# Optimization experiments

Hardware: AMD Instinct MI355X
Metric: run time of the kernel (lower is better)

The kernel has to match this reference:

```python
import jax, jax.numpy as jnp
import numpy as np

E, H, I, G, T, TOPK = 8, 2048, 5632, 128, 256, 2
FP8_MAX = 448.0


def setup_inputs() -> dict:
    key = jax.random.key(0)
    ks = jax.random.split(key, 8)
    hidden_states = jax.random.normal(ks[0], (T, H), jnp.float32)
    router_logits = jax.random.normal(ks[1], (T, E), jnp.float32)
    # unpacked INT4 values in [-8, 7], stored as int8 (modeling unpack_int4->int8)
    w3w1_q = jax.random.randint(ks[2], (E, H, 2 * I), -8, 8, dtype=jnp.int32).astype(jnp.int8)
    w2_q = jax.random.randint(ks[3], (E, I, H), -8, 8, dtype=jnp.int32).astype(jnp.int8)
    # group-wise weight scales: [in_dim/G, out_dim] per expert
    w3w1_scale = jax.random.uniform(ks[4], (E, H // G, 2 * I), jnp.float32, 0.005, 0.02)
    w2_scale = jax.random.uniform(ks[5], (E, I // G, H), jnp.float32, 0.005, 0.02)
    # per-expert static activation scales (p3_p1 = max(p1,p3) pre-folded)
    input_scale_fc1 = jax.random.uniform(ks[6], (E,), jnp.float32, 0.5, 1.5)
    input_scale_fc2 = jax.random.uniform(ks[7], (E,), jnp.float32, 0.5, 1.5)
    return dict(hidden_states=hidden_states, router_logits=router_logits,
                w3w1_q=w3w1_q, w2_q=w2_q, w3w1_scale=w3w1_scale, w2_scale=w2_scale,
                input_scale_fc1=input_scale_fc1, input_scale_fc2=input_scale_fc2)


def _fp8_qdq(x, s):
    # quantize activation to fp8_e4m3 (clamp + round-to-fp8) then dequantize
    q = jnp.clip(x / s, -FP8_MAX, FP8_MAX).astype(jnp.float8_e4m3fn)
    return q.astype(jnp.float32)


def _dequant(w_q, w_scale):
    # w_q: [in, out] int8; w_scale: [in/G, out] -> repeat each group G rows
    return w_q.astype(jnp.float32) * jnp.repeat(w_scale, G, axis=0)


def _routing(router_logits):
    probs = jax.nn.softmax(router_logits, axis=-1)            # [T, E]
    vals, idx = jax.lax.top_k(probs, TOPK)                    # [T, K]
    scales = vals / jnp.sum(vals, axis=-1, keepdims=True)     # renormalize
    # per-token gate weight for every expert, zero if not selected: [T, E]
    gate = jnp.sum(jax.nn.one_hot(idx, E, dtype=scales.dtype) * scales[..., None], axis=1)
    return gate


def reference(hidden_states, router_logits, w3w1_q, w2_q, w3w1_scale, w2_scale,
              input_scale_fc1, input_scale_fc2):
    gate = _routing(router_logits)                            # [T, E]
    out = jnp.zeros_like(hidden_states)
    for e in range(E):  # fixed small expert loop (structurally distinct weights)
        s1 = input_scale_fc1[e]
        act = _fp8_qdq(hidden_states, s1)                     # [T, H]
        w_fc1 = _dequant(w3w1_q[e], w3w1_scale[e])            # [H, 2I]
        fc1 = (act @ w_fc1) * s1                              # [T, 2I]
        up, gt = fc1[:, :I], fc1[:, I:]                       # chunk: (w3 | w1)
        h = up * jax.nn.silu(gt)                              # [T, I]
        s2 = input_scale_fc2[e]
        act2 = _fp8_qdq(h, s2)
        w_fc2 = _dequant(w2_q[e], w2_scale[e])                # [I, H]
        fc2 = (act2 @ w_fc2) * s2                             # [T, H]
        out = out + fc2 * gate[:, e:e + 1]
    return out
```

## Files before the change

### kernel.cpp

```cpp
#include <hip/hip_runtime.h>
#include <hip/hip_bf16.h>
#include <hip/hip_fp8.h>
#include <cstdint>
#include <cstddef>

#define E_ 8
#define H_ 2048
#define I_ 5632
#define N1_ (2 * I_)
#define G_ 128
#define T_ 256
#define RPE 256
#define SLOTS (E_ * RPE)

typedef __attribute__((ext_vector_type(4))) float f32x4;
typedef __attribute__((ext_vector_type(8))) __bf16 bf16x8;
typedef __attribute__((ext_vector_type(2))) int i32x2;

#define WS_CNT 0
#define WS_TOKEN 64
#define WS_GATE (64 + SLOTS * 4)
#define WS_A1 32768
#define WS_A2 (WS_A1 + SLOTS * H_ * 2)

__device__ __forceinline__ uint32_t pack_bf16x2(float a, float b) {
  union { float f; uint32_t u; } ua, ub;
  ua.f = a; ub.f = b;
  uint32_t ra = (ua.u + 0x7FFFu + ((ua.u >> 16) & 1u)) >> 16;
  uint32_t rb = (ub.u + 0x7FFFu + ((ub.u >> 16) & 1u)) & 0xFFFF0000u;
  return ra | rb;
}

__device__ __forceinline__ float fp8_qdq1(float x) {
  x = fminf(fmaxf(x, -448.0f), 448.0f);
  __hip_fp8_e4m3 q(x);
  return (float)q;
}

__device__ __forceinline__ void block_sync_nodrain() {
  __builtin_amdgcn_sched_barrier(0);
  asm volatile("s_waitcnt lgkmcnt(0)" ::: "memory");
  __builtin_amdgcn_s_barrier();
  __builtin_amdgcn_sched_barrier(0);
}

__device__ __forceinline__ void wissue(const int* __restrict__ wpt, size_t ldN, int m,
                                       i32x2 wv[4]) {
#pragma unroll
  for (int c = 0; c < 4; ++c)
    wv[c] = __builtin_nontemporal_load(
        reinterpret_cast<const i32x2*>(wpt + ((size_t)m * 32 + c) * ldN));
}

__device__ __forceinline__ void wstage(__hip_bfloat16 (*Btb)[64][8], int kqw, int n0, int h4,
                                       const i32x2 wv[4], float2 sc) {
  uint32_t a0 = pack_bf16x2((float)wv[0].x * sc.x, (float)wv[1].x * sc.x);
  uint32_t a1 = pack_bf16x2((float)wv[2].x * sc.x, (float)wv[3].x * sc.x);
  uint32_t b0 = pack_bf16x2((float)wv[0].y * sc.y, (float)wv[1].y * sc.y);
  uint32_t b1 = pack_bf16x2((float)wv[2].y * sc.y, (float)wv[3].y * sc.y);
  *(uint2*)&Btb[kqw][n0][h4] = make_uint2(a0, a1);
  *(uint2*)&Btb[kqw][n0 + 1][h4] = make_uint2(b0, b1);
}

__device__ __forceinline__ void aissue(const __hip_bfloat16* const aptr[4], int m, int nact,
                                       uint4 av[4]) {
#pragma unroll
  for (int mj = 0; mj < 4; ++mj)
    if (mj < nact) av[mj] = *(const uint4*)(aptr[mj] + (size_t)m * 32);
}

__device__ __forceinline__ void do_mfma(const __hip_bfloat16 (*Btb)[64][8], int kq, int lm,
                                        int nact, const uint4 afr[4], f32x4 acc[4][4]) {
#pragma unroll
  for (int f = 0; f < 4; ++f) {
    union { uint4 u; bf16x8 v; } bu;
    bu.u = *(const uint4*)&Btb[kq][f * 16 + lm][0];
#pragma unroll
    for (int mj = 0; mj < 4; ++mj)
      if (mj < nact) {
        union { uint4 u; bf16x8 v; } au;
        au.u = afr[mj];
        acc[mj][f] = __builtin_amdgcn_mfma_f32_16x16x32_bf16(au.v, bu.v, acc[mj][f], 0, 0, 0);
      }
  }
}

__global__ void routing_kernel(const float* __restrict__ logits,
                               int* __restrict__ cnt,
                               int* __restrict__ token_of, float* __restrict__ gate_of) {
  __shared__ int s_cnt[E_];
  int t = threadIdx.x;
  if (t < E_) s_cnt[t] = 0;
  __syncthreads();
  float l[E_];
#pragma unroll
  for (int e = 0; e < E_; e++) l[e] = logits[t * E_ + e];
  int i0 = 0;
#pragma unroll
  for (int e = 1; e < E_; e++) if (l[e] > l[i0]) i0 = e;
  int i1 = (i0 == 0) ? 1 : 0;
#pragma unroll
  for (int e = 0; e < E_; e++) if (e != i0 && l[e] > l[i1]) i1 = e;
  float g0 = 1.0f / (1.0f + expf(l[i1] - l[i0]));
  float g1 = 1.0f - g0;
  int s0 = atomicAdd(&s_cnt[i0], 1);
  int s1 = atomicAdd(&s_cnt[i1], 1);
  token_of[i0 * RPE + s0] = t;  gate_of[i0 * RPE + s0] = g0;
  token_of[i1 * RPE + s1] = t;  gate_of[i1 * RPE + s1] = g1;
  __syncthreads();
  if (t < E_) cnt[t] = s_cnt[t];
  for (int idx = t; idx < SLOTS; idx += 256) {
    int e = idx >> 8, r = idx & (RPE - 1);
    if (r >= s_cnt[e]) { token_of[idx] = 0; gate_of[idx] = 0.0f; }
  }
}

__global__ void gather_kernel(const float* __restrict__ hidden,
                              const float* __restrict__ is1,
                              const int* __restrict__ cnt,
                              const int* __restrict__ token_of,
                              __hip_bfloat16* __restrict__ A1) {
  int sg = blockIdx.x;
  int e = sg >> 8, r = sg & (RPE - 1);
  bool pad = (r >= cnt[e]);
  uint4 u;
  if (pad) {
    u.x = u.y = u.z = u.w = 0u;
  } else {
    int t = token_of[sg];
    float s1 = is1[e];
    const float4* hp = (const float4*)(hidden + (size_t)t * H_ + threadIdx.x * 8);
    float4 x0 = hp[0], x1 = hp[1];
    float q0 = fp8_qdq1(x0.x / s1), q1 = fp8_qdq1(x0.y / s1);
    float q2 = fp8_qdq1(x0.z / s1), q3 = fp8_qdq1(x0.w / s1);
    float q4 = fp8_qdq1(x1.x / s1), q5 = fp8_qdq1(x1.y / s1);
    float q6 = fp8_qdq1(x1.z / s1), q7 = fp8_qdq1(x1.w / s1);
    u.x = pack_bf16x2(q0, q1); u.y = pack_bf16x2(q2, q3);
    u.z = pack_bf16x2(q4, q5); u.w = pack_bf16x2(q6, q7);
  }
  ((uint4*)(A1 + (size_t)sg * H_))[threadIdx.x] = u;
}

__global__ __launch_bounds__(256) void fc1_kernel(
    const int* __restrict__ w1, const float* __restrict__ w1s,
    const float* __restrict__ is1v, const float* __restrict__ is2v,
    const int* __restrict__ cnt,
    const __hip_bfloat16* __restrict__ A1, __hip_bfloat16* __restrict__ A2) {
  __shared__ __hip_bfloat16 Bt[2][4][64][8];
  const int e = blockIdx.y;
  const int j0 = blockIdx.x * 32;
  const int tid = threadIdx.x;
  const int wave = tid >> 6, lane = tid & 63;
  const int lm = lane & 15, kq = lane >> 4;
  const int np = tid & 31, kg = tid >> 5;
  const int kqw = kg >> 1, h4 = (kg & 1) * 4;
  const int n0s = np * 2;
  const int gc2 = (n0s < 32) ? (j0 + n0s) : (I_ + j0 + (n0s - 32));
  const int* wpt = w1 + (size_t)e * H_ * N1_ + (size_t)(kg * 4) * N1_ + gc2;
  const float* spt = w1s + (size_t)e * (H_ / G_) * N1_ + gc2;
  const __hip_bfloat16* abase = A1 + (size_t)e * RPE * H_;

  const int C16 = (cnt[e] + 15) >> 4;
  int nact = (C16 - wave + 3) >> 2;
  if (nact < 0) nact = 0;

  f32x4 acc[4][4];
#pragma unroll
  for (int a = 0; a < 4; a++)
#pragma unroll
    for (int b = 0; b < 4; b++) acc[a][b] = (f32x4){0.f, 0.f, 0.f, 0.f};

  const __hip_bfloat16* aptr[4];
#pragma unroll
  for (int mj = 0; mj < 4; mj++)
    aptr[mj] = abase + (size_t)((mj * 4 + wave) * 16 + lm) * H_ + kq * 8;

  i32x2 wv0[4], wv1[4];
  uint4 av0[4], av1[4];
  float2 sc0 = *(const float2*)spt;
  float2 sc1 = sc0;
  wissue(wpt, N1_, 0, wv0);
  wissue(wpt, N1_, 1, wv1);
  aissue(aptr, 0, nact, av1);
  wstage(Bt[0], kqw, n0s, h4, wv0, sc0);
  block_sync_nodrain();

  for (int i = 0; i < 31; ++i) {
    const int ks = 2 * i;
    if (((ks + 2) & 3) == 0) sc0 = *(const float2*)(spt + (size_t)((ks + 2) >> 2) * N1_);
    wissue(wpt, N1_, ks + 2, wv0);
    aissue(aptr, ks + 1, nact, av0);
    do_mfma(Bt[0], kq, lm, nact, av1, acc);
    wstage(Bt[1], kqw, n0s, h4, wv1, sc1);
    block_sync_nodrain();
    if (((ks + 3) & 3) == 1) sc1 = *(const float2*)(spt + (size_t)((ks + 3) >> 2) * N1_);
    wissue(wpt, N1_, ks + 3, wv1);
    aissue(aptr, ks + 2, nact, av1);
    do_mfma(Bt[1], kq, lm, nact, av0, acc);
    wstage(Bt[0], kqw, n0s, h4, wv0, sc0);
    block_sync_nodrain();
  }
  aissue(aptr, 63, nact, av0);
  do_mfma(Bt[0], kq, lm, nact, av1, acc);
  wstage(Bt[1], kqw, n0s, h4, wv1, sc1);
  block_sync_nodrain();
  do_mfma(Bt[1], kq, lm, nact, av0, acc);

  const float s1 = is1v[e], s2 = is2v[e];
  __hip_bfloat16* a2base = A2 + (size_t)(e * RPE) * I_ + j0;
#pragma unroll
  for (int mj = 0; mj < 4; mj++) {
    if (mj < nact) {
      int mrow = (mj * 4 + wave) * 16 + kq * 4;
#pragma unroll
      for (int r = 0; r < 4; r++) {
#pragma unroll
        for (int f = 0; f < 2; f++) {
          float up = acc[mj][f][r] * s1;
          float gt = acc[mj][f + 2][r] * s1;
          float h = up * (gt / (1.0f + expf(-gt)));
          float q = fp8_qdq1(h / s2);
          a2base[(size_t)(mrow + r) * I_ + f * 16 + lm] = __float2bfloat16(q);
        }
      }
    }
  }
}

__global__ __launch_bounds__(256) void fc2_kernel(
    const int* __restrict__ w2, const float* __restrict__ w2s,
    const float* __restrict__ is2v, const int* __restrict__ cnt,
    const int* __restrict__ token_of, const float* __restrict__ gate_of,
    const __hip_bfloat16* __restrict__ A2, float* __restrict__ out) {
  __shared__ __hip_bfloat16 Bt[2][4][64][8];
  const int e = blockIdx.y;
  const int n0 = blockIdx.x * 64;
  const int z = blockIdx.z;
  const int tid = threadIdx.x;
  const int wave = tid >> 6, lane = tid & 63;
  const int lm = lane & 15, kq = lane >> 4;
  const int np = tid & 31, kg = tid >> 5;
  const int kqw = kg >> 1, h4 = (kg & 1) * 4;
  const int n0s = np * 2;
  const int gc2 = n0 + n0s;
  const int z11 = z * 11;
  const int* wpt = w2 + (size_t)e * I_ * H_ + (size_t)(z * 44 * 32 + kg * 4) * H_ + gc2;
  const float* spt = w2s + (size_t)e * (I_ / G_) * H_ + gc2;
  const __hip_bfloat16* abase = A2 + (size_t)e * RPE * I_;

  const int c_n = cnt[e];
  const int C16 = (c_n + 15) >> 4;
  int nact = (C16 - wave + 3) >> 2;
  if (nact < 0) nact = 0;

  f32x4 acc[4][4];
#pragma unroll
  for (int a = 0; a < 4; a++)
#pragma unroll
    for (int b = 0; b < 4; b++) acc[a][b] = (f32x4){0.f, 0.f, 0.f, 0.f};

  const __hip_bfloat16* aptr[4];
#pragma unroll
  for (int mj = 0; mj < 4; mj++)
    aptr[mj] = abase + (size_t)((mj * 4 + wave) * 16 + lm) * I_ + (size_t)z * 44 * 32 + kq * 8;

  i32x2 wv0[4], wv1[4];
  uint4 av0[4], av1[4];
  float2 sc0 = *(const float2*)(spt + (size_t)z11 * H_);
  float2 sc1 = sc0;
  wissue(wpt, H_, 0, wv0);
  wissue(wpt, H_, 1, wv1);
  aissue(aptr, 0, nact, av1);
  wstage(Bt[0], kqw, n0s, h4, wv0, sc0);
  block_sync_nodrain();

  for (int i = 0; i < 21; ++i) {
    const int ks = 2 * i;
    if (((ks + 2) & 3) == 0)
      sc0 = *(const float2*)(spt + (size_t)(z11 + ((ks + 2) >> 2)) * H_);
    wissue(wpt, H_, ks + 2, wv0);
    aissue(aptr, ks + 1, nact, av0);
    do_mfma(Bt[0], kq, lm, nact, av1, acc);
    wstage(Bt[1], kqw, n0s, h4, wv1, sc1);
    block_sync_nodrain();
    if (((ks + 3) & 3) == 1)
      sc1 = *(const float2*)(spt + (size_t)(z11 + ((ks + 3) >> 2)) * H_);
    wissue(wpt, H_, ks + 3, wv1);
    aissue(aptr, ks + 2, nact, av1);
    do_mfma(Bt[1], kq, lm, nact, av0, acc);
    wstage(Bt[0], kqw, n0s, h4, wv0, sc0);
    block_sync_nodrain();
  }
  aissue(aptr, 43, nact, av0);
  do_mfma(Bt[0], kq, lm, nact, av1, acc);
  wstage(Bt[1], kqw, n0s, h4, wv1, sc1);
  block_sync_nodrain();
  do_mfma(Bt[1], kq, lm, nact, av0, acc);

  const float s2 = is2v[e];
#pragma unroll
  for (int mj = 0; mj < 4; mj++) {
    if (mj < nact) {
      int sl0 = (mj * 4 + wave) * 16 + kq * 4;
#pragma unroll
      for (int r = 0; r < 4; r++) {
        int slot = sl0 + r;
        if (slot < c_n) {
          int t = token_of[e * RPE + slot];
          float gv = gate_of[e * RPE + slot] * s2;
#pragma unroll
          for (int f = 0; f < 4; f++)
            atomicAdd(out + (size_t)t * H_ + n0 + f * 16 + lm, acc[mj][f][r] * gv);
        }
      }
    }
  }
}

extern "C" void kernel_launch(void* const* d_in, const int* in_sizes, int n_in,
                              void* d_out, int out_size, void* d_ws, size_t ws_size,
                              hipStream_t stream) {
  const float* hidden = (const float*)d_in[0];
  const float* logits = (const float*)d_in[1];
  const int* w1 = (const int*)d_in[2];
  const int* w2 = (const int*)d_in[3];
  const float* w1s = (const float*)d_in[4];
  const float* w2s = (const float*)d_in[5];
  const float* is1 = (const float*)d_in[6];
  const float* is2 = (const float*)d_in[7];
  float* out = (float*)d_out;
  char* ws = (char*)d_ws;
  int* cnt = (int*)(ws + WS_CNT);
  int* token_of = (int*)(ws + WS_TOKEN);
  float* gate_of = (float*)(ws + WS_GATE);
  __hip_bfloat16* A1 = (__hip_bfloat16*)(ws + WS_A1);
  __hip_bfloat16* A2 = (__hip_bfloat16*)(ws + WS_A2);

  hipMemsetAsync(d_out, 0, (size_t)T_ * H_ * sizeof(float), stream);
  routing_kernel<<<1, 256, 0, stream>>>(logits, cnt, token_of, gate_of);
  gather_kernel<<<SLOTS, 256, 0, stream>>>(hidden, is1, cnt, token_of, A1);
  fc1_kernel<<<dim3(I_ / 32, E_), 256, 0, stream>>>(w1, w1s, is1, is2, cnt, A1, A2);
  fc2_kernel<<<dim3(H_ / 64, E_, 4), 256, 0, stream>>>(w2, w2s, is2, cnt, token_of,
                                                       gate_of, A2, out);
}
```

Measured before the change: 1.242 ms.

## Give each wave its own weight tile to drop block barriers in FC kernels

The FC1 and FC2 kernels are restructured so each wave dequantizes and stages its own private slice of weight columns (16-byte loads, per-wave LDS buffers) and covers all token rows itself. This removes the block-wide barriers in the K loop and doubles the columns per block. The aim is to cut barrier stalls and improve weight load width. In exchange, A loads are repeated across waves and register pressure rises with 8x2 accumulators. The gather kernel also skips writing padded rows beyond the last 16-row tile.

```diff
diff --git a/kernel.cpp b/kernel.cpp
--- a/kernel.cpp
+++ b/kernel.cpp
@@ -15,7 +15,7 @@
 
 typedef __attribute__((ext_vector_type(4))) float f32x4;
 typedef __attribute__((ext_vector_type(8))) __bf16 bf16x8;
-typedef __attribute__((ext_vector_type(2))) int i32x2;
+typedef __attribute__((ext_vector_type(4))) int i32x4;
 
 #define WS_CNT 0
 #define WS_TOKEN 64
@@ -37,49 +37,42 @@
   return (float)q;
 }
 
-__device__ __forceinline__ void block_sync_nodrain() {
-  __builtin_amdgcn_sched_barrier(0);
-  asm volatile("s_waitcnt lgkmcnt(0)" ::: "memory");
-  __builtin_amdgcn_s_barrier();
-  __builtin_amdgcn_sched_barrier(0);
-}
-
-__device__ __forceinline__ void wissue(const int* __restrict__ wpt, size_t ldN, int m,
-                                       i32x2 wv[4]) {
+__device__ __forceinline__ void wissue4(const int* __restrict__ wpt, size_t ldN, int m,
+                                        i32x4 wv[4]) {
 #pragma unroll
   for (int c = 0; c < 4; ++c)
     wv[c] = __builtin_nontemporal_load(
-        reinterpret_cast<const i32x2*>(wpt + ((size_t)m * 32 + c) * ldN));
-}
-
-__device__ __forceinline__ void wstage(__hip_bfloat16 (*Btb)[64][8], int kqw, int n0, int h4,
-                                       const i32x2 wv[4], float2 sc) {
-  uint32_t a0 = pack_bf16x2((float)wv[0].x * sc.x, (float)wv[1].x * sc.x);
-  uint32_t a1 = pack_bf16x2((float)wv[2].x * sc.x, (float)wv[3].x * sc.x);
-  uint32_t b0 = pack_bf16x2((float)wv[0].y * sc.y, (float)wv[1].y * sc.y);
-  uint32_t b1 = pack_bf16x2((float)wv[2].y * sc.y, (float)wv[3].y * sc.y);
-  *(uint2*)&Btb[kqw][n0][h4] = make_uint2(a0, a1);
-  *(uint2*)&Btb[kqw][n0 + 1][h4] = make_uint2(b0, b1);
-}
-
-__device__ __forceinline__ void aissue(const __hip_bfloat16* const aptr[4], int m, int nact,
-                                       uint4 av[4]) {
-#pragma unroll
-  for (int mj = 0; mj < 4; ++mj)
+        reinterpret_cast<const i32x4*>(wpt + ((size_t)m * 32 + c) * ldN));
+}
+
+__device__ __forceinline__ void wstage4(__hip_bfloat16 (*Btb)[32][8], int kqw, int c4, int s0,
+                                        const i32x4 wv[4], f32x4 sc) {
+#pragma unroll
+  for (int i = 0; i < 4; ++i) {
+    uint32_t p0 = pack_bf16x2((float)wv[0][i] * sc[i], (float)wv[1][i] * sc[i]);
+    uint32_t p1 = pack_bf16x2((float)wv[2][i] * sc[i], (float)wv[3][i] * sc[i]);
+    *(uint2*)&Btb[kqw][c4 + i][s0] = make_uint2(p0, p1);
+  }
+}
+
+__device__ __forceinline__ void aissue8(const __hip_bfloat16* const aptr[8], int m, int nact,
+                                        uint4 av[8]) {
+#pragma unroll
+  for (int mj = 0; mj < 8; ++mj)
     if (mj < nact) av[mj] = *(const uint4*)(aptr[mj] + (size_t)m * 32);
 }
 
-__device__ __forceinline__ void do_mfma(const __hip_bfloat16 (*Btb)[64][8], int kq, int lm,
-                                        int nact, const uint4 afr[4], f32x4 acc[4][4]) {
-#pragma unroll
-  for (int f = 0; f < 4; ++f) {
+__device__ __forceinline__ void mfma2x8(const __hip_bfloat16 (*Btb)[32][8], int kq, int lm,
+                                        int nact, const uint4 av[8], f32x4 acc[8][2]) {
+#pragma unroll
+  for (int f = 0; f < 2; ++f) {
     union { uint4 u; bf16x8 v; } bu;
     bu.u = *(const uint4*)&Btb[kq][f * 16 + lm][0];
 #pragma unroll
-    for (int mj = 0; mj < 4; ++mj)
+    for (int mj = 0; mj < 8; ++mj)
       if (mj < nact) {
         union { uint4 u; bf16x8 v; } au;
-        au.u = afr[mj];
+        au.u = av[mj];
         acc[mj][f] = __builtin_amdgcn_mfma_f32_16x16x32_bf16(au.v, bu.v, acc[mj][f], 0, 0, 0);
       }
   }
@@ -122,7 +115,10 @@
                               __hip_bfloat16* __restrict__ A1) {
   int sg = blockIdx.x;
   int e = sg >> 8, r = sg & (RPE - 1);
-  bool pad = (r >= cnt[e]);
+  int c_n = cnt[e];
+  int lim = ((c_n + 15) >> 4) << 4;
+  if (r >= lim) return;
+  bool pad = (r >= c_n);
   uint4 u;
   if (pad) {
     u.x = u.y = u.z = u.w = 0u;
@@ -141,176 +137,170 @@
   ((uint4*)(A1 + (size_t)sg * H_))[threadIdx.x] = u;
 }
 
-__global__ __launch_bounds__(256) void fc1_kernel(
+__global__ __launch_bounds__(256, 2) void fc1_kernel(
     const int* __restrict__ w1, const float* __restrict__ w1s,
     const float* __restrict__ is1v, const float* __restrict__ is2v,
     const int* __restrict__ cnt,
     const __hip_bfloat16* __restrict__ A1, __hip_bfloat16* __restrict__ A2) {
-  __shared__ __hip_bfloat16 Bt[2][4][64][8];
+  __shared__ __hip_bfloat16 Bt[4][2][4][32][8];
   const int e = blockIdx.y;
-  const int j0 = blockIdx.x * 32;
+  const int j0 = blockIdx.x * 64;
   const int tid = threadIdx.x;
   const int wave = tid >> 6, lane = tid & 63;
   const int lm = lane & 15, kq = lane >> 4;
-  const int np = tid & 31, kg = tid >> 5;
-  const int kqw = kg >> 1, h4 = (kg & 1) * 4;
-  const int n0s = np * 2;
-  const int gc2 = (n0s < 32) ? (j0 + n0s) : (I_ + j0 + (n0s - 32));
-  const int* wpt = w1 + (size_t)e * H_ * N1_ + (size_t)(kg * 4) * N1_ + gc2;
-  const float* spt = w1s + (size_t)e * (H_ / G_) * N1_ + gc2;
+  const int c4 = (lane & 7) * 4;
+  const int kq4 = lane >> 3;
+  const int kqw = kq4 >> 1, s0 = (kq4 & 1) * 4;
+  const int gc4 = (c4 < 16) ? (j0 + wave * 16 + c4) : (I_ + j0 + wave * 16 + (c4 - 16));
+  const int* wpt = w1 + (size_t)e * H_ * N1_ + (size_t)(kq4 * 4) * N1_ + gc4;
+  const float* spt = w1s + (size_t)e * (H_ / G_) * N1_ + gc4;
   const __hip_bfloat16* abase = A1 + (size_t)e * RPE * H_;
+  auto& Btw = Bt[wave];
 
   const int C16 = (cnt[e] + 15) >> 4;
-  int nact = (C16 - wave + 3) >> 2;
-  if (nact < 0) nact = 0;
-
-  f32x4 acc[4][4];
-#pragma unroll
-  for (int a = 0; a < 4; a++)
-#pragma unroll
-    for (int b = 0; b < 4; b++) acc[a][b] = (f32x4){0.f, 0.f, 0.f, 0.f};
-
-  const __hip_bfloat16* aptr[4];
-#pragma unroll
-  for (int mj = 0; mj < 4; mj++)
-    aptr[mj] = abase + (size_t)((mj * 4 + wave) * 16 + lm) * H_ + kq * 8;
-
-  i32x2 wv0[4], wv1[4];
-  uint4 av0[4], av1[4];
-  float2 sc0 = *(const float2*)spt;
-  float2 sc1 = sc0;
-  wissue(wpt, N1_, 0, wv0);
-  wissue(wpt, N1_, 1, wv1);
-  aissue(aptr, 0, nact, av1);
-  wstage(Bt[0], kqw, n0s, h4, wv0, sc0);
-  block_sync_nodrain();
-
-  for (int i = 0; i < 31; ++i) {
-    const int ks = 2 * i;
-    if (((ks + 2) & 3) == 0) sc0 = *(const float2*)(spt + (size_t)((ks + 2) >> 2) * N1_);
-    wissue(wpt, N1_, ks + 2, wv0);
-    aissue(aptr, ks + 1, nact, av0);
-    do_mfma(Bt[0], kq, lm, nact, av1, acc);
-    wstage(Bt[1], kqw, n0s, h4, wv1, sc1);
-    block_sync_nodrain();
-    if (((ks + 3) & 3) == 1) sc1 = *(const float2*)(spt + (size_t)((ks + 3) >> 2) * N1_);
-    wissue(wpt, N1_, ks + 3, wv1);
-    aissue(aptr, ks + 2, nact, av1);
-    do_mfma(Bt[1], kq, lm, nact, av0, acc);
-    wstage(Bt[0], kqw, n0s, h4, wv0, sc0);
-    block_sync_nodrain();
-  }
-  aissue(aptr, 63, nact, av0);
-  do_mfma(Bt[0], kq, lm, nact, av1, acc);
-  wstage(Bt[1], kqw, n0s, h4, wv1, sc1);
-  block_sync_nodrain();
-  do_mfma(Bt[1], kq, lm, nact, av0, acc);
-
   const float s1 = is1v[e], s2 = is2v[e];
-  __hip_bfloat16* a2base = A2 + (size_t)(e * RPE) * I_ + j0;
-#pragma unroll
-  for (int mj = 0; mj < 4; mj++) {
-    if (mj < nact) {
-      int mrow = (mj * 4 + wave) * 16 + kq * 4;
-#pragma unroll
-      for (int r = 0; r < 4; r++) {
-#pragma unroll
-        for (int f = 0; f < 2; f++) {
-          float up = acc[mj][f][r] * s1;
-          float gt = acc[mj][f + 2][r] * s1;
+  __hip_bfloat16* a2base = A2 + (size_t)(e * RPE) * I_ + j0 + wave * 16;
+
+  for (int mb = 0; mb < C16; mb += 8) {
+    const int nact = (C16 - mb < 8) ? (C16 - mb) : 8;
+    const __hip_bfloat16* aptr[8];
+#pragma unroll
+    for (int mj = 0; mj < 8; ++mj)
+      aptr[mj] = abase + (size_t)((mb + mj) * 16 + lm) * H_ + kq * 8;
+
+    f32x4 acc[8][2];
+#pragma unroll
+    for (int a = 0; a < 8; ++a)
+#pragma unroll
+      for (int b = 0; b < 2; ++b) acc[a][b] = (f32x4){0.f, 0.f, 0.f, 0.f};
+
+    i32x4 wv0[4], wv1[4];
+    uint4 av0[8], av1[8];
+    f32x4 sc0 = *(const f32x4*)spt;
+    f32x4 sc1 = sc0;
+    wissue4(wpt, N1_, 0, wv0);
+    wissue4(wpt, N1_, 1, wv1);
+    aissue8(aptr, 0, nact, av1);
+    wstage4(&Btw[0][0], kqw, c4, s0, wv0, sc0);
+
+    for (int i = 0; i < 31; ++i) {
+      const int m = 2 * i;
+      if (((m + 2) & 3) == 0) sc0 = *(const f32x4*)(spt + (size_t)((m + 2) >> 2) * N1_);
+      wissue4(wpt, N1_, m + 2, wv0);
+      aissue8(aptr, m + 1, nact, av0);
+      mfma2x8(&Btw[0][0], kq, lm, nact, av1, acc);
+      wstage4(&Btw[1][0], kqw, c4, s0, wv1, sc1);
+      if (((m + 3) & 3) == 1) sc1 = *(const f32x4*)(spt + (size_t)((m + 3) >> 2) * N1_);
+      wissue4(wpt, N1_, m + 3, wv1);
+      aissue8(aptr, m + 2, nact, av1);
+      mfma2x8(&Btw[1][0], kq, lm, nact, av0, acc);
+      wstage4(&Btw[0][0], kqw, c4, s0, wv0, sc0);
+    }
+    aissue8(aptr, 63, nact, av0);
+    mfma2x8(&Btw[0][0], kq, lm, nact, av1, acc);
+    wstage4(&Btw[1][0], kqw, c4, s0, wv1, sc1);
+    mfma2x8(&Btw[1][0], kq, lm, nact, av0, acc);
+
+#pragma unroll
+    for (int mj = 0; mj < 8; ++mj) {
+      if (mj < nact) {
+        int mrow = (mb + mj) * 16 + kq * 4;
+#pragma unroll
+        for (int r = 0; r < 4; ++r) {
+          float up = acc[mj][0][r] * s1;
+          float gt = acc[mj][1][r] * s1;
           float h = up * (gt / (1.0f + expf(-gt)));
           float q = fp8_qdq1(h / s2);
-          a2base[(size_t)(mrow + r) * I_ + f * 16 + lm] = __float2bfloat16(q);
+          a2base[(size_t)(mrow + r) * I_ + lm] = __float2bfloat16(q);
         }
       }
     }
   }
 }
 
-__global__ __launch_bounds__(256) void fc2_kernel(
+__global__ __launch_bounds__(256, 2) void fc2_kernel(
     const int* __restrict__ w2, const float* __restrict__ w2s,
     const float* __restrict__ is2v, const int* __restrict__ cnt,
     const int* __restrict__ token_of, const float* __restrict__ gate_of,
     const __hip_bfloat16* __restrict__ A2, float* __restrict__ out) {
-  __shared__ __hip_bfloat16 Bt[2][4][64][8];
+  __shared__ __hip_bfloat16 Bt[4][2][4][32][8];
   const int e = blockIdx.y;
-  const int n0 = blockIdx.x * 64;
+  const int n0 = blockIdx.x * 128;
   const int z = blockIdx.z;
   const int tid = threadIdx.x;
   const int wave = tid >> 6, lane = tid & 63;
   const int lm = lane & 15, kq = lane >> 4;
-  const int np = tid & 31, kg = tid >> 5;
-  const int kqw = kg >> 1, h4 = (kg & 1) * 4;
-  const int n0s = np * 2;
-  const int gc2 = n0 + n0s;
-  const int z11 = z * 11;
-  const int* wpt = w2 + (size_t)e * I_ * H_ + (size_t)(z * 44 * 32 + kg * 4) * H_ + gc2;
-  const float* spt = w2s + (size_t)e * (I_ / G_) * H_ + gc2;
-  const __hip_bfloat16* abase = A2 + (size_t)e * RPE * I_;
+  const int c4 = (lane & 7) * 4;
+  const int kq4 = lane >> 3;
+  const int kqw = kq4 >> 1, s0 = (kq4 & 1) * 4;
+  const int gc4 = n0 + wave * 32 + c4;
+  const int* wpt = w2 + (size_t)e * I_ * H_ + (size_t)(z * 1408 + kq4 * 4) * H_ + gc4;
+  const float* spt = w2s + (size_t)e * (I_ / G_) * H_ + gc4;
+  const __hip_bfloat16* abase = A2 + (size_t)e * RPE * I_ + z * 1408;
+  auto& Btw = Bt[wave];
 
   const int c_n = cnt[e];
   const int C16 = (c_n + 15) >> 4;
-  int nact = (C16 - wave + 3) >> 2;
-  if (nact < 0) nact = 0;
-
-  f32x4 acc[4][4];
-#pragma unroll
-  for (int a = 0; a < 4; a++)
-#pragma unroll
-    for (int b = 0; b < 4; b++) acc[a][b] = (f32x4){0.f, 0.f, 0.f, 0.f};
-
-  const __hip_bfloat16* aptr[4];
-#pragma unroll
-  for (int mj = 0; mj < 4; mj++)
-    aptr[mj] = abase + (size_t)((mj * 4 + wave) * 16 + lm) * I_ + (size_t)z * 44 * 32 + kq * 8;
-
-  i32x2 wv0[4], wv1[4];
-  uint4 av0[4], av1[4];
-  float2 sc0 = *(const float2*)(spt + (size_t)z11 * H_);
-  float2 sc1 = sc0;
-  wissue(wpt, H_, 0, wv0);
-  wissue(wpt, H_, 1, wv1);
-  aissue(aptr, 0, nact, av1);
-  wstage(Bt[0], kqw, n0s, h4, wv0, sc0);
-  block_sync_nodrain();
-
-  for (int i = 0; i < 21; ++i) {
-    const int ks = 2 * i;
-    if (((ks + 2) & 3) == 0)
-      sc0 = *(const float2*)(spt + (size_t)(z11 + ((ks + 2) >> 2)) * H_);
-    wissue(wpt, H_, ks + 2, wv0);
-    aissue(aptr, ks + 1, nact, av0);
-    do_mfma(Bt[0], kq, lm, nact, av1, acc);
-    wstage(Bt[1], kqw, n0s, h4, wv1, sc1);
-    block_sync_nodrain();
-    if (((ks + 3) & 3) == 1)
-      sc1 = *(const float2*)(spt + (size_t)(z11 + ((ks + 3) >> 2)) * H_);
-    wissue(wpt, H_, ks + 3, wv1);
-    aissue(aptr, ks + 2, nact, av1);
-    do_mfma(Bt[1], kq, lm, nact, av0, acc);
-    wstage(Bt[0], kqw, n0s, h4, wv0, sc0);
-    block_sync_nodrain();
-  }
-  aissue(aptr, 43, nact, av0);
-  do_mfma(Bt[0], kq, lm, nact, av1, acc);
-  wstage(Bt[1], kqw, n0s, h4, wv1, sc1);
-  block_sync_nodrain();
-  do_mfma(Bt[1], kq, lm, nact, av0, acc);
-
+  const int z11 = z * 11;
   const float s2 = is2v[e];
-#pragma unroll
-  for (int mj = 0; mj < 4; mj++) {
-    if (mj < nact) {
-      int sl0 = (mj * 4 + wave) * 16 + kq * 4;
-#pragma unroll
-      for (int r = 0; r < 4; r++) {
-        int slot = sl0 + r;
-        if (slot < c_n) {
-          int t = token_of[e * RPE + slot];
-          float gv = gate_of[e * RPE + slot] * s2;
-#pragma unroll
-          for (int f = 0; f < 4; f++)
-            atomicAdd(out + (size_t)t * H_ + n0 + f * 16 + lm, acc[mj][f][r] * gv);
+
+  for (int mb = 0; mb < C16; mb += 8) {
+    const int nact = (C16 - mb < 8) ? (C16 - mb) : 8;
+    const __hip_bfloat16* aptr[8];
+#pragma unroll
+    for (int mj = 0; mj < 8; ++mj)
+      aptr[mj] = abase + (size_t)((mb + mj) * 16 + lm) * I_ + kq * 8;
+
+    f32x4 acc[8][2];
+#pragma unroll
+    for (int a = 0; a < 8; ++a)
+#pragma unroll
+      for (int b = 0; b < 2; ++b) acc[a][b] = (f32x4){0.f, 0.f, 0.f, 0.f};
+
+    i32x4 wv0[4], wv1[4];
+    uint4 av0[8], av1[8];
+    f32x4 sc0 = *(const f32x4*)(spt + (size_t)z11 * H_);
+    f32x4 sc1 = sc0;
+    wissue4(wpt, H_, 0, wv0);
+    wissue4(wpt, H_, 1, wv1);
+    aissue8(aptr, 0, nact, av1);
+    wstage4(&Btw[0][0], kqw, c4, s0, wv0, sc0);
+
+    for (int i = 0; i < 21; ++i) {
+      const int m = 2 * i;
+      if (((m + 2) & 3) == 0)
+        sc0 = *(const f32x4*)(spt + (size_t)(z11 + ((m + 2) >> 2)) * H_);
+      wissue4(wpt, H_, m + 2, wv0);
+      aissue8(aptr, m + 1, nact, av0);
+      mfma2x8(&Btw[0][0], kq, lm, nact, av1, acc);
+      wstage4(&Btw[1][0], kqw, c4, s0, wv1, sc1);
+      if (((m + 3) & 3) == 1)
+        sc1 = *(const f32x4*)(spt + (size_t)(z11 + ((m + 3) >> 2)) * H_);
+      wissue4(wpt, H_, m + 3, wv1);
+      aissue8(aptr, m + 2, nact, av1);
+      mfma2x8(&Btw[1][0], kq, lm, nact, av0, acc);
+      wstage4(&Btw[0][0], kqw, c4, s0, wv0, sc0);
+    }
+    aissue8(aptr, 43, nact, av0);
+    mfma2x8(&Btw[0][0], kq, lm, nact, av1, acc);
+    wstage4(&Btw[1][0], kqw, c4, s0, wv1, sc1);
+    mfma2x8(&Btw[1][0], kq, lm, nact, av0, acc);
+
+#pragma unroll
+    for (int mj = 0; mj < 8; ++mj) {
+      if (mj < nact) {
+        int sl0 = (mb + mj) * 16 + kq * 4;
+#pragma unroll
+        for (int r = 0; r < 4; ++r) {
+          int slot = sl0 + r;
+          if (slot < c_n) {
+            int t = token_of[e * RPE + slot];
+            float gv = gate_of[e * RPE + slot] * s2;
+#pragma unroll
+            for (int f = 0; f < 2; ++f)
+              atomicAdd(out + (size_t)t * H_ + n0 + wave * 32 + f * 16 + lm,
+                        acc[mj][f][r] * gv);
+          }
         }
       }
     }
@@ -339,7 +329,7 @@
   hipMemsetAsync(d_out, 0, (size_t)T_ * H_ * sizeof(float), stream);
   routing_kernel<<<1, 256, 0, stream>>>(logits, cnt, token_of, gate_of);
   gather_kernel<<<SLOTS, 256, 0, stream>>>(hidden, is1, cnt, token_of, A1);
-  fc1_kernel<<<dim3(I_ / 32, E_), 256, 0, stream>>>(w1, w1s, is1, is2, cnt, A1, A2);
-  fc2_kernel<<<dim3(H_ / 64, E_, 4), 256, 0, stream>>>(w2, w2s, is2, cnt, token_of,
-                                                       gate_of, A2, out);
-}
+  fc1_kernel<<<dim3(I_ / 64, E_), 256, 0, stream>>>(w1, w1s, is1, is2, cnt, A1, A2);
+  fc2_kernel<<<dim3(H_ / 128, E_, 4), 256, 0, stream>>>(w2, w2s, is2, cnt, token_of,
+                                                        gate_of, A2, out);
+}
```

Result: slower. 1.326 ms (+6.7%).

## Widen weight loads to 16 bytes and deepen weight prefetch to four stages

Applied to the files above, without the earlier changes.

In fc1 and fc2, each thread now loads four adjacent int32 weight columns per row as 128-bit nontemporal loads over two rows, replacing the earlier 64-bit loads over four rows. The k-loop is unrolled by four with four register buffers, so weight loads are issued about four k-steps before they are used and the group scale is loaded once per group as a float4. The aim is fewer, wider memory requests and more loads in flight, which should hide HBM latency on this weight-bandwidth-bound GEMM. The gather kernel also returns early for padded rows past the 16-aligned count, skipping writes that are never read. The cost is higher register pressure from the extra buffers and a new LDS store pattern that writes 32-bit elements, which may cause bank conflicts.

```diff
diff --git a/kernel.cpp b/kernel.cpp
--- a/kernel.cpp
+++ b/kernel.cpp
@@ -15,7 +15,7 @@
 
 typedef __attribute__((ext_vector_type(4))) float f32x4;
 typedef __attribute__((ext_vector_type(8))) __bf16 bf16x8;
-typedef __attribute__((ext_vector_type(2))) int i32x2;
+typedef __attribute__((ext_vector_type(4))) int i32x4;
 
 #define WS_CNT 0
 #define WS_TOKEN 64
@@ -45,21 +45,20 @@
 }
 
 __device__ __forceinline__ void wissue(const int* __restrict__ wpt, size_t ldN, int m,
-                                       i32x2 wv[4]) {
-#pragma unroll
-  for (int c = 0; c < 4; ++c)
-    wv[c] = __builtin_nontemporal_load(
-        reinterpret_cast<const i32x2*>(wpt + ((size_t)m * 32 + c) * ldN));
-}
-
-__device__ __forceinline__ void wstage(__hip_bfloat16 (*Btb)[64][8], int kqw, int n0, int h4,
-                                       const i32x2 wv[4], float2 sc) {
-  uint32_t a0 = pack_bf16x2((float)wv[0].x * sc.x, (float)wv[1].x * sc.x);
-  uint32_t a1 = pack_bf16x2((float)wv[2].x * sc.x, (float)wv[3].x * sc.x);
-  uint32_t b0 = pack_bf16x2((float)wv[0].y * sc.y, (float)wv[1].y * sc.y);
-  uint32_t b1 = pack_bf16x2((float)wv[2].y * sc.y, (float)wv[3].y * sc.y);
-  *(uint2*)&Btb[kqw][n0][h4] = make_uint2(a0, a1);
-  *(uint2*)&Btb[kqw][n0 + 1][h4] = make_uint2(b0, b1);
+                                       i32x4 wv[2]) {
+  wv[0] = __builtin_nontemporal_load(
+      reinterpret_cast<const i32x4*>(wpt + ((size_t)m * 32) * ldN));
+  wv[1] = __builtin_nontemporal_load(
+      reinterpret_cast<const i32x4*>(wpt + ((size_t)m * 32 + 1) * ldN));
+}
+
+__device__ __forceinline__ void wstage(__hip_bfloat16 (*Btb)[64][8], int kqs, int c4, int s0,
+                                       const i32x4 wv[2], f32x4 sc) {
+#pragma unroll
+  for (int i = 0; i < 4; ++i) {
+    uint32_t p = pack_bf16x2((float)wv[0][i] * sc[i], (float)wv[1][i] * sc[i]);
+    *(uint32_t*)&Btb[kqs][c4 + i][s0] = p;
+  }
 }
 
 __device__ __forceinline__ void aissue(const __hip_bfloat16* const aptr[4], int m, int nact,
@@ -122,7 +121,10 @@
                               __hip_bfloat16* __restrict__ A1) {
   int sg = blockIdx.x;
   int e = sg >> 8, r = sg & (RPE - 1);
-  bool pad = (r >= cnt[e]);
+  int c_n = cnt[e];
+  int lim = ((c_n + 15) >> 4) << 4;
+  if (r >= lim) return;
+  bool pad = (r >= c_n);
   uint4 u;
   if (pad) {
     u.x = u.y = u.z = u.w = 0u;
@@ -152,12 +154,12 @@
   const int tid = threadIdx.x;
   const int wave = tid >> 6, lane = tid & 63;
   const int lm = lane & 15, kq = lane >> 4;
-  const int np = tid & 31, kg = tid >> 5;
-  const int kqw = kg >> 1, h4 = (kg & 1) * 4;
-  const int n0s = np * 2;
-  const int gc2 = (n0s < 32) ? (j0 + n0s) : (I_ + j0 + (n0s - 32));
-  const int* wpt = w1 + (size_t)e * H_ * N1_ + (size_t)(kg * 4) * N1_ + gc2;
-  const float* spt = w1s + (size_t)e * (H_ / G_) * N1_ + gc2;
+  const int c4 = (tid & 15) * 4;
+  const int r2 = tid >> 4;
+  const int kqs = r2 >> 2, s0 = (r2 * 2) & 7;
+  const int gc4 = (c4 < 32) ? (j0 + c4) : (I_ + j0 + (c4 - 32));
+  const int* wpt = w1 + (size_t)e * H_ * N1_ + (size_t)(r2 * 2) * N1_ + gc4;
+  const float* spt = w1s + (size_t)e * (H_ / G_) * N1_ + gc4;
   const __hip_bfloat16* abase = A1 + (size_t)e * RPE * H_;
 
   const int C16 = (cnt[e] + 15) >> 4;
@@ -175,36 +177,43 @@
   for (int mj = 0; mj < 4; mj++)
     aptr[mj] = abase + (size_t)((mj * 4 + wave) * 16 + lm) * H_ + kq * 8;
 
-  i32x2 wv0[4], wv1[4];
+  i32x4 wvA[2], wvB[2], wvC[2], wvD[2];
   uint4 av0[4], av1[4];
-  float2 sc0 = *(const float2*)spt;
-  float2 sc1 = sc0;
-  wissue(wpt, N1_, 0, wv0);
-  wissue(wpt, N1_, 1, wv1);
+  f32x4 scCur = *(const f32x4*)spt;
+  wissue(wpt, N1_, 0, wvA);
+  wissue(wpt, N1_, 1, wvB);
+  wissue(wpt, N1_, 2, wvC);
+  wissue(wpt, N1_, 3, wvD);
   aissue(aptr, 0, nact, av1);
-  wstage(Bt[0], kqw, n0s, h4, wv0, sc0);
+  wstage(Bt[0], kqs, c4, s0, wvA, scCur);
   block_sync_nodrain();
 
-  for (int i = 0; i < 31; ++i) {
-    const int ks = 2 * i;
-    if (((ks + 2) & 3) == 0) sc0 = *(const float2*)(spt + (size_t)((ks + 2) >> 2) * N1_);
-    wissue(wpt, N1_, ks + 2, wv0);
-    aissue(aptr, ks + 1, nact, av0);
+  for (int it = 0; it < 16; ++it) {
+    const int m = it * 4;
+    f32x4 scN = scCur;
+    if (it + 1 < 16) scN = *(const f32x4*)(spt + (size_t)(it + 1) * N1_);
+    if (m + 4 < 64) wissue(wpt, N1_, m + 4, wvA);
+    if (m + 1 < 64) aissue(aptr, m + 1, nact, av0);
     do_mfma(Bt[0], kq, lm, nact, av1, acc);
-    wstage(Bt[1], kqw, n0s, h4, wv1, sc1);
-    block_sync_nodrain();
-    if (((ks + 3) & 3) == 1) sc1 = *(const float2*)(spt + (size_t)((ks + 3) >> 2) * N1_);
-    wissue(wpt, N1_, ks + 3, wv1);
-    aissue(aptr, ks + 2, nact, av1);
+    wstage(Bt[1], kqs, c4, s0, wvB, scCur);
+    block_sync_nodrain();
+    if (m + 5 < 64) wissue(wpt, N1_, m + 5, wvB);
+    if (m + 2 < 64) aissue(aptr, m + 2, nact, av1);
     do_mfma(Bt[1], kq, lm, nact, av0, acc);
-    wstage(Bt[0], kqw, n0s, h4, wv0, sc0);
-    block_sync_nodrain();
-  }
-  aissue(aptr, 63, nact, av0);
-  do_mfma(Bt[0], kq, lm, nact, av1, acc);
-  wstage(Bt[1], kqw, n0s, h4, wv1, sc1);
-  block_sync_nodrain();
-  do_mfma(Bt[1], kq, lm, nact, av0, acc);
+    wstage(Bt[0], kqs, c4, s0, wvC, scCur);
+    block_sync_nodrain();
+    if (m + 6 < 64) wissue(wpt, N1_, m + 6, wvC);
+    if (m + 3 < 64) aissue(aptr, m + 3, nact, av0);
+    do_mfma(Bt[0], kq, lm, nact, av1, acc);
+    wstage(Bt[1], kqs, c4, s0, wvD, scCur);
+    block_sync_nodrain();
+    if (m + 7 < 64) wissue(wpt, N1_, m + 7, wvD);
+    if (m + 4 < 64) aissue(aptr, m + 4, nact, av1);
+    do_mfma(Bt[1], kq, lm, nact, av0, acc);
+    if (m + 4 < 64) wstage(Bt[0], kqs, c4, s0, wvA, scN);
+    block_sync_nodrain();
+    scCur = scN;
+  }
 
   const float s1 = is1v[e], s2 = is2v[e];
   __hip_bfloat16* a2base = A2 + (size_t)(e * RPE) * I_ + j0;
@@ -239,14 +248,14 @@
   const int tid = threadIdx.x;
   const int wave = tid >> 6, lane = tid & 63;
   const int lm = lane & 15, kq = lane >> 4;
-  const int np = tid & 31, kg = tid >> 5;
-  const int kqw = kg >> 1, h4 = (kg & 1) * 4;
-  const int n0s = np * 2;
-  const int gc2 = n0 + n0s;
+  const int c4 = (tid & 15) * 4;
+  const int r2 = tid >> 4;
+  const int kqs = r2 >> 2, s0 = (r2 * 2) & 7;
+  const int gc4 = n0 + c4;
   const int z11 = z * 11;
-  const int* wpt = w2 + (size_t)e * I_ * H_ + (size_t)(z * 44 * 32 + kg * 4) * H_ + gc2;
-  const float* spt = w2s + (size_t)e * (I_ / G_) * H_ + gc2;
-  const __hip_bfloat16* abase = A2 + (size_t)e * RPE * I_;
+  const int* wpt = w2 + (size_t)e * I_ * H_ + (size_t)(z * 1408 + r2 * 2) * H_ + gc4;
+  const float* spt = w2s + (size_t)e * (I_ / G_) * H_ + gc4;
+  const __hip_bfloat16* abase = A2 + (size_t)e * RPE * I_ + z * 1408;
 
   const int c_n = cnt[e];
   const int C16 = (c_n + 15) >> 4;
@@ -262,40 +271,45 @@
   const __hip_bfloat16* aptr[4];
 #pragma unroll
   for (int mj = 0; mj < 4; mj++)
-    aptr[mj] = abase + (size_t)((mj * 4 + wave) * 16 + lm) * I_ + (size_t)z * 44 * 32 + kq * 8;
-
-  i32x2 wv0[4], wv1[4];
+    aptr[mj] = abase + (size_t)((mj * 4 + wave) * 16 + lm) * I_ + kq * 8;
+
+  i32x4 wvA[2], wvB[2], wvC[2], wvD[2];
   uint4 av0[4], av1[4];
-  float2 sc0 = *(const float2*)(spt + (size_t)z11 * H_);
-  float2 sc1 = sc0;
-  wissue(wpt, H_, 0, wv0);
-  wissue(wpt, H_, 1, wv1);
+  f32x4 scCur = *(const f32x4*)(spt + (size_t)z11 * H_);
+  wissue(wpt, H_, 0, wvA);
+  wissue(wpt, H_, 1, wvB);
+  wissue(wpt, H_, 2, wvC);
+  wissue(wpt, H_, 3, wvD);
   aissue(aptr, 0, nact, av1);
-  wstage(Bt[0], kqw, n0s, h4, wv0, sc0);
+  wstage(Bt[0], kqs, c4, s0, wvA, scCur);
   block_sync_nodrain();
 
-  for (int i = 0; i < 21; ++i) {
-    const int ks = 2 * i;
-    if (((ks + 2) & 3) == 0)
-      sc0 = *(const float2*)(spt + (size_t)(z11 + ((ks + 2) >> 2)) * H_);
-    wissue(wpt, H_, ks + 2, wv0);
-    aissue(aptr, ks + 1, nact, av0);
+  for (int it = 0; it < 11; ++it) {
+    const int m = it * 4;
+    f32x4 scN = scCur;
+    if (it + 1 < 11) scN = *(const f32x4*)(spt + (size_t)(z11 + it + 1) * H_);
+    if (m + 4 < 44) wissue(wpt, H_, m + 4, wvA);
+    if (m + 1 < 44) aissue(aptr, m + 1, nact, av0);
     do_mfma(Bt[0], kq, lm, nact, av1, acc);
-    wstage(Bt[1], kqw, n0s, h4, wv1, sc1);
-    block_sync_nodrain();
-    if (((ks + 3) & 3) == 1)
-      sc1 = *(const float2*)(spt + (size_t)(z11 + ((ks + 3) >> 2)) * H_);
-    wissue(wpt, H_, ks + 3, wv1);
-    aissue(aptr, ks + 2, nact, av1);
+    wstage(Bt[1], kqs, c4, s0, wvB, scCur);
+    block_sync_nodrain();
+    if (m + 5 < 44) wissue(wpt, H_, m + 5, wvB);
+    if (m + 2 < 44) aissue(aptr, m + 2, nact, av1);
     do_mfma(Bt[1], kq, lm, nact, av0, acc);
-    wstage(Bt[0], kqw, n0s, h4, wv0, sc0);
-    block_sync_nodrain();
-  }
-  aissue(aptr, 43, nact, av0);
-  do_mfma(Bt[0], kq, lm, nact, av1, acc);
-  wstage(Bt[1], kqw, n0s, h4, wv1, sc1);
-  block_sync_nodrain();
-  do_mfma(Bt[1], kq, lm, nact, av0, acc);
+    wstage(Bt[0], kqs, c4, s0, wvC, scCur);
+    block_sync_nodrain();
+    if (m + 6 < 44) wissue(wpt, H_, m + 6, wvC);
+    if (m + 3 < 44) aissue(aptr, m + 3, nact, av0);
+    do_mfma(Bt[0], kq, lm, nact, av1, acc);
+    wstage(Bt[1], kqs, c4, s0, wvD, scCur);
+    block_sync_nodrain();
+    if (m + 7 < 44) wissue(wpt, H_, m + 7, wvD);
+    if (m + 4 < 44) aissue(aptr, m + 4, nact, av1);
+    do_mfma(Bt[1], kq, lm, nact, av0, acc);
+    if (m + 4 < 44) wstage(Bt[0], kqs, c4, s0, wvA, scN);
+    block_sync_nodrain();
+    scCur = scN;
+  }
 
   const float s2 = is2v[e];
 #pragma unroll
```

After: 1.269 ms. 2.1% more time.
